# Kernel tuning notes

Measured on AMD Instinct MI355X. Metric: run time of the kernel, lower is better.

The kernel has to match this reference:

```python
import jax, jax.numpy as jnp
import numpy as np

N, D, C, P = 4096, 512, 100, 64
EPS_COS = 1e-8   # torch cosine_similarity norm clamp
EPS_INV = 1e-5   # module's 1/(d + 1e-5)


def setup_inputs() -> dict:
    key = jax.random.key(0)
    k1, k2, k3, k4 = jax.random.split(key, 4)
    feats = jax.random.normal(k1, (N, D), dtype=jnp.float32)
    protos = jax.random.normal(k2, (C, P, D), dtype=jnp.float32)
    cls_ids = jax.random.randint(k3, (N,), 0, C)
    proto_labels = jax.random.randint(k4, (C, P), 0, 1000)
    return {"feats": feats, "protos": protos, "cls_ids": cls_ids,
            "proto_labels": proto_labels}


def reference(feats, protos, cls_ids, proto_labels):
    # Gather each box's class-conditional prototype set: [N, P, D]
    p = protos[cls_ids]
    pl = proto_labels[cls_ids]                       # [N, P]

    # cosine distance: 1 - f.p / (max(|f|,eps) * max(|p|,eps))
    dot = jnp.einsum('nd,npd->np', feats, p)         # [N, P]
    fnorm = jnp.maximum(jnp.linalg.norm(feats, axis=-1, keepdims=True), EPS_COS)
    pnorm = jnp.maximum(jnp.linalg.norm(p, axis=-1), EPS_COS)
    d_cos = 1.0 - dot / (fnorm * pnorm)

    diff = feats[:, None, :] - p                     # [N, P, D]
    d_l1 = jnp.mean(jnp.abs(diff), axis=-1)          # F.l1_loss (mean)
    d_l2 = jnp.mean(diff * diff, axis=-1)            # F.mse_loss (mean)

    dists = jnp.stack([d_cos, d_l1, d_l2], axis=1)   # [N, 3, P]
    probs = jax.nn.softmax(1.0 / (dists + EPS_INV), axis=-1).mean(axis=1)  # [N, P]

    idx = jnp.argmax(probs, axis=-1)                 # [N]
    labels = jnp.take_along_axis(pl, idx[:, None], axis=1)[:, 0]
    return labels, probs
```

## Files before the change

kernel.cpp:

```cpp
#include <hip/hip_runtime.h>

#define D 512
#define P 64
#define WPB 4
#define EPS_COS 1e-8f
#define EPS_INV 1e-5f

__device__ __forceinline__ float wave_sum(float v) {
#pragma unroll
    for (int m = 32; m >= 1; m >>= 1) v += __shfl_xor(v, m, 64);
    return v;
}

__global__ __launch_bounds__(256) void proto_norm_kernel(
    const float* __restrict__ protos, float* __restrict__ pp, int rows)
{
    const int lane = threadIdx.x & 63;
    const int wave = threadIdx.x >> 6;
    const int r = blockIdx.x * WPB + wave;
    if (r >= rows) return;
    const float* row = protos + (size_t)r * D;
    const float4 a = *(const float4*)(row + lane * 4);
    const float4 b = *(const float4*)(row + 256 + lane * 4);
    float s = a.x*a.x + a.y*a.y + a.z*a.z + a.w*a.w
            + b.x*b.x + b.y*b.y + b.z*b.z + b.w*b.w;
    s = wave_sum(s);
    if (lane == 0) pp[r] = s;
}

__global__ __launch_bounds__(WPB * 64) void proto_probs_kernel(
    const float* __restrict__ feats,
    const float* __restrict__ protos,
    const int*   __restrict__ cls_ids,
    const int*   __restrict__ proto_labels,
    const float* __restrict__ ppbuf,
    float* __restrict__ out,
    int N)
{
    const int lane = threadIdx.x & 63;
    const int wave = threadIdx.x >> 6;
    const int n = blockIdx.x * WPB + wave;
    if (n >= N) return;

    const int cls = cls_ids[n];
    const float* f  = feats  + (size_t)n * D;
    const float* pr = protos + (size_t)cls * (P * D);

    const float4 f0 = *(const float4*)(f + lane * 4);
    const float4 f1 = *(const float4*)(f + 256 + lane * 4);

    float ff = f0.x*f0.x + f0.y*f0.y + f0.z*f0.z + f0.w*f0.w
             + f1.x*f1.x + f1.y*f1.y + f1.z*f1.z + f1.w*f1.w;
    ff = wave_sum(ff);

    const int jsel = (lane >> 3) & 7;
    const int gown = lane & 7;
    const bool hi32 = (lane & 32) != 0;
    const bool hi16 = (lane & 16) != 0;
    const bool hi8  = (lane & 8)  != 0;

    float r_dot = 0.f, r_l1 = 0.f;

    for (int g = 0; g < 8; ++g) {
        float pd[8], pl[8];
#pragma unroll
        for (int j = 0; j < 8; ++j) {
            const float* row = pr + (size_t)(8 * g + j) * D;
            const float4 q0 = *(const float4*)(row + lane * 4);
            const float4 q1 = *(const float4*)(row + 256 + lane * 4);
            float dot, l1, t;
            dot  = f0.x*q0.x; t = f0.x - q0.x; l1  = fabsf(t);
            dot += f0.y*q0.y; t = f0.y - q0.y; l1 += fabsf(t);
            dot += f0.z*q0.z; t = f0.z - q0.z; l1 += fabsf(t);
            dot += f0.w*q0.w; t = f0.w - q0.w; l1 += fabsf(t);
            dot += f1.x*q1.x; t = f1.x - q1.x; l1 += fabsf(t);
            dot += f1.y*q1.y; t = f1.y - q1.y; l1 += fabsf(t);
            dot += f1.z*q1.z; t = f1.z - q1.z; l1 += fabsf(t);
            dot += f1.w*q1.w; t = f1.w - q1.w; l1 += fabsf(t);
            pd[j] = dot; pl[j] = l1;
        }
#pragma unroll
        for (int k = 0; k < 4; ++k) {
            const float sd = hi32 ? pd[k] : pd[k + 4];
            const float sl = hi32 ? pl[k] : pl[k + 4];
            const float rd = __shfl_xor(sd, 32, 64);
            const float rl = __shfl_xor(sl, 32, 64);
            pd[k] = (hi32 ? pd[k + 4] : pd[k]) + rd;
            pl[k] = (hi32 ? pl[k + 4] : pl[k]) + rl;
        }
#pragma unroll
        for (int k = 0; k < 2; ++k) {
            const float sd = hi16 ? pd[k] : pd[k + 2];
            const float sl = hi16 ? pl[k] : pl[k + 2];
            const float rd = __shfl_xor(sd, 16, 64);
            const float rl = __shfl_xor(sl, 16, 64);
            pd[k] = (hi16 ? pd[k + 2] : pd[k]) + rd;
            pl[k] = (hi16 ? pl[k + 2] : pl[k]) + rl;
        }
        {
            const float sd = hi8 ? pd[0] : pd[1];
            const float sl = hi8 ? pl[0] : pl[1];
            const float rd = __shfl_xor(sd, 8, 64);
            const float rl = __shfl_xor(sl, 8, 64);
            pd[0] = (hi8 ? pd[1] : pd[0]) + rd;
            pl[0] = (hi8 ? pl[1] : pl[0]) + rl;
        }
#pragma unroll
        for (int m = 4; m >= 1; m >>= 1) {
            pd[0] += __shfl_xor(pd[0], m, 64);
            pl[0] += __shfl_xor(pl[0], m, 64);
        }
        if (gown == g) { r_dot = pd[0]; r_l1 = pl[0]; }
    }

    const int myp = 8 * gown + jsel;
    const float s_pp = ppbuf[cls * P + myp];

    const float fnorm = fmaxf(sqrtf(ff),   EPS_COS);
    const float pnorm = fmaxf(sqrtf(s_pp), EPS_COS);
    const float d_cos = 1.0f - r_dot / (fnorm * pnorm);
    const float d_l1  = r_l1 * (1.0f / (float)D);
    const float d_l2  = (ff - 2.0f * r_dot + s_pp) * (1.0f / (float)D);

    float s[3];
    s[0] = 1.0f / (d_cos + EPS_INV);
    s[1] = 1.0f / (d_l1  + EPS_INV);
    s[2] = 1.0f / (d_l2  + EPS_INV);

    float prob = 0.f;
#pragma unroll
    for (int i = 0; i < 3; ++i) {
        float m = s[i];
#pragma unroll
        for (int w = 32; w >= 1; w >>= 1) m = fmaxf(m, __shfl_xor(m, w, 64));
        const float e = expf(s[i] - m);
        const float denom = wave_sum(e);
        prob += e / denom;
    }
    prob *= (1.0f / 3.0f);

    float best = prob;
    int   bidx = myp;
#pragma unroll
    for (int w = 32; w >= 1; w >>= 1) {
        const float ov = __shfl_xor(best, w, 64);
        const int   oi = __shfl_xor(bidx, w, 64);
        if (ov > best || (ov == best && oi < bidx)) { best = ov; bidx = oi; }
    }

    out[(size_t)N + (size_t)n * P + myp] = prob;
    if (lane == 0) {
        out[n] = (float)proto_labels[cls * P + bidx];
    }
}

extern "C" void kernel_launch(void* const* d_in, const int* in_sizes, int n_in,
                              void* d_out, int out_size, void* d_ws, size_t ws_size,
                              hipStream_t stream) {
    const float* feats        = (const float*)d_in[0];
    const float* protos       = (const float*)d_in[1];
    const int*   cls_ids      = (const int*)d_in[2];
    const int*   proto_labels = (const int*)d_in[3];
    float* out = (float*)d_out;
    float* pp  = (float*)d_ws;

    const int N    = in_sizes[2];
    const int rows = in_sizes[1] / D;

    proto_norm_kernel<<<(rows + WPB - 1) / WPB, WPB * 64, 0, stream>>>(
        protos, pp, rows);
    proto_probs_kernel<<<(N + WPB - 1) / WPB, WPB * 64, 0, stream>>>(
        feats, protos, cls_ids, proto_labels, pp, out, N);
}
```

Baseline: 104.3 us.

## Bucket boxes by class and share prototype tiles in LDS across boxes

Adds a histogram, scan and scatter pipeline that groups boxes by class into chunks of up to 16. Each block then stages that class's 64 prototypes into shared memory in two passes and has each wave process 4 boxes against the staged tile, so every prototype load is reused 16 times instead of being re-read per box. The cost is four extra small launches, atomics and a 64 KB LDS tile per block, which limits occupancy. Chunks with fewer than 16 boxes leave some waves computing on padding, and the descriptor grid is fixed at 512 blocks.

```diff
diff --git a/kernel.cpp b/kernel.cpp
--- a/kernel.cpp
+++ b/kernel.cpp
@@ -2,10 +2,12 @@
 
 #define D 512
 #define P 64
-#define WPB 4
+#define CHUNK 16
+#define MAXDESC 512
 #define EPS_COS 1e-8f
 #define EPS_INV 1e-5f
 
+
 __device__ __forceinline__ float wave_sum(float v) {
 #pragma unroll
     for (int m = 32; m >= 1; m >>= 1) v += __shfl_xor(v, m, 64);
@@ -16,8 +18,7 @@
     const float* __restrict__ protos, float* __restrict__ pp, int rows)
 {
     const int lane = threadIdx.x & 63;
-    const int wave = threadIdx.x >> 6;
-    const int r = blockIdx.x * WPB + wave;
+    const int r = blockIdx.x * 4 + (threadIdx.x >> 6);
     if (r >= rows) return;
     const float* row = protos + (size_t)r * D;
     const float4 a = *(const float4*)(row + lane * 4);
@@ -28,129 +29,222 @@
     if (lane == 0) pp[r] = s;
 }
 
-__global__ __launch_bounds__(WPB * 64) void proto_probs_kernel(
+__global__ __launch_bounds__(256) void hist_kernel(
+    const int* __restrict__ cls, int* counts, int N)
+{
+    const int n = blockIdx.x * 256 + threadIdx.x;
+    if (n < N) atomicAdd(&counts[cls[n]], 1);
+}
+
+__global__ __launch_bounds__(64) void scan_desc_kernel(
+    const int* __restrict__ counts, int* base, int* desc, int* ndesc, int C)
+{
+    const int lane = threadIdx.x;
+    const int c0 = lane, c1 = lane + 64;
+    const int v0 = (c0 < C) ? counts[c0] : 0;
+    const int v1 = (c1 < C) ? counts[c1] : 0;
+    int s0 = v0, s1 = v1;
+#pragma unroll
+    for (int d = 1; d < 64; d <<= 1) {
+        int t = __shfl_up(s0, d, 64); if (lane >= d) s0 += t;
+        t     = __shfl_up(s1, d, 64); if (lane >= d) s1 += t;
+    }
+    s1 += __shfl(s0, 63, 64);
+    const int b0 = s0 - v0, b1 = s1 - v1;
+    if (c0 < C) base[c0] = b0;
+    if (c1 < C) base[c1] = b1;
+
+    const int g0 = (v0 + CHUNK - 1) / CHUNK, g1 = (v1 + CHUNK - 1) / CHUNK;
+    int t0 = g0, t1 = g1;
+#pragma unroll
+    for (int d = 1; d < 64; d <<= 1) {
+        int t = __shfl_up(t0, d, 64); if (lane >= d) t0 += t;
+        t     = __shfl_up(t1, d, 64); if (lane >= d) t1 += t;
+    }
+    t1 += __shfl(t0, 63, 64);
+    const int go0 = t0 - g0, go1 = t1 - g1;
+    if (lane == 63) ndesc[0] = t1;
+    for (int k = 0; k < g0; ++k) {
+        const int di = go0 + k;
+        desc[3*di] = c0; desc[3*di+1] = b0 + CHUNK*k; desc[3*di+2] = min(CHUNK, v0 - CHUNK*k);
+    }
+    for (int k = 0; k < g1; ++k) {
+        const int di = go1 + k;
+        desc[3*di] = c1; desc[3*di+1] = b1 + CHUNK*k; desc[3*di+2] = min(CHUNK, v1 - CHUNK*k);
+    }
+}
+
+__global__ __launch_bounds__(256) void scatter_kernel(
+    const int* __restrict__ cls, const int* __restrict__ base,
+    int* fill, int* sorted, int N)
+{
+    const int n = blockIdx.x * 256 + threadIdx.x;
+    if (n < N) {
+        const int c = cls[n];
+        const int pos = base[c] + atomicAdd(&fill[c], 1);
+        sorted[pos] = n;
+    }
+}
+
+__global__ __launch_bounds__(256, 2) void proto_main_kernel(
     const float* __restrict__ feats,
     const float* __restrict__ protos,
-    const int*   __restrict__ cls_ids,
     const int*   __restrict__ proto_labels,
     const float* __restrict__ ppbuf,
-    float* __restrict__ out,
-    int N)
-{
+    const int*   __restrict__ sorted,
+    const int*   __restrict__ desc,
+    const int*   __restrict__ ndesc,
+    float* __restrict__ out, int N)
+{
+    __shared__ float tile[32 * D];
+    const int nd = ndesc[0];
+    if ((int)blockIdx.x >= nd) return;
+    const int cls   = desc[3*blockIdx.x];
+    const int start = desc[3*blockIdx.x+1];
+    const int cnt   = desc[3*blockIdx.x+2];
     const int lane = threadIdx.x & 63;
     const int wave = threadIdx.x >> 6;
-    const int n = blockIdx.x * WPB + wave;
-    if (n >= N) return;
-
-    const int cls = cls_ids[n];
-    const float* f  = feats  + (size_t)n * D;
+
+    int  nidx[4];
+    bool valid[4];
+#pragma unroll
+    for (int k = 0; k < 4; ++k) {
+        const int pos = wave + 4*k;
+        valid[k] = pos < cnt;
+        nidx[k]  = sorted[start + (valid[k] ? pos : (cnt - 1))];
+    }
+
+    float4 f0[4], f1[4];
+    float  ff[4];
+#pragma unroll
+    for (int b = 0; b < 4; ++b) {
+        const float* f = feats + (size_t)nidx[b] * D;
+        f0[b] = *(const float4*)(f + lane * 4);
+        f1[b] = *(const float4*)(f + 256 + lane * 4);
+        float s = f0[b].x*f0[b].x + f0[b].y*f0[b].y + f0[b].z*f0[b].z + f0[b].w*f0[b].w
+                + f1[b].x*f1[b].x + f1[b].y*f1[b].y + f1[b].z*f1[b].z + f1[b].w*f1[b].w;
+        ff[b] = wave_sum(s);
+    }
+
     const float* pr = protos + (size_t)cls * (P * D);
-
-    const float4 f0 = *(const float4*)(f + lane * 4);
-    const float4 f1 = *(const float4*)(f + 256 + lane * 4);
-
-    float ff = f0.x*f0.x + f0.y*f0.y + f0.z*f0.z + f0.w*f0.w
-             + f1.x*f1.x + f1.y*f1.y + f1.z*f1.z + f1.w*f1.w;
-    ff = wave_sum(ff);
-
     const int jsel = (lane >> 3) & 7;
     const int gown = lane & 7;
     const bool hi32 = (lane & 32) != 0;
     const bool hi16 = (lane & 16) != 0;
     const bool hi8  = (lane & 8)  != 0;
 
-    float r_dot = 0.f, r_l1 = 0.f;
-
-    for (int g = 0; g < 8; ++g) {
-        float pd[8], pl[8];
-#pragma unroll
-        for (int j = 0; j < 8; ++j) {
-            const float* row = pr + (size_t)(8 * g + j) * D;
-            const float4 q0 = *(const float4*)(row + lane * 4);
-            const float4 q1 = *(const float4*)(row + 256 + lane * 4);
-            float dot, l1, t;
-            dot  = f0.x*q0.x; t = f0.x - q0.x; l1  = fabsf(t);
-            dot += f0.y*q0.y; t = f0.y - q0.y; l1 += fabsf(t);
-            dot += f0.z*q0.z; t = f0.z - q0.z; l1 += fabsf(t);
-            dot += f0.w*q0.w; t = f0.w - q0.w; l1 += fabsf(t);
-            dot += f1.x*q1.x; t = f1.x - q1.x; l1 += fabsf(t);
-            dot += f1.y*q1.y; t = f1.y - q1.y; l1 += fabsf(t);
-            dot += f1.z*q1.z; t = f1.z - q1.z; l1 += fabsf(t);
-            dot += f1.w*q1.w; t = f1.w - q1.w; l1 += fabsf(t);
-            pd[j] = dot; pl[j] = l1;
-        }
-#pragma unroll
-        for (int k = 0; k < 4; ++k) {
-            const float sd = hi32 ? pd[k] : pd[k + 4];
-            const float sl = hi32 ? pl[k] : pl[k + 4];
-            const float rd = __shfl_xor(sd, 32, 64);
-            const float rl = __shfl_xor(sl, 32, 64);
-            pd[k] = (hi32 ? pd[k + 4] : pd[k]) + rd;
-            pl[k] = (hi32 ? pl[k + 4] : pl[k]) + rl;
-        }
-#pragma unroll
-        for (int k = 0; k < 2; ++k) {
-            const float sd = hi16 ? pd[k] : pd[k + 2];
-            const float sl = hi16 ? pl[k] : pl[k + 2];
-            const float rd = __shfl_xor(sd, 16, 64);
-            const float rl = __shfl_xor(sl, 16, 64);
-            pd[k] = (hi16 ? pd[k + 2] : pd[k]) + rd;
-            pl[k] = (hi16 ? pl[k + 2] : pl[k]) + rl;
-        }
-        {
-            const float sd = hi8 ? pd[0] : pd[1];
-            const float sl = hi8 ? pl[0] : pl[1];
-            const float rd = __shfl_xor(sd, 8, 64);
-            const float rl = __shfl_xor(sl, 8, 64);
-            pd[0] = (hi8 ? pd[1] : pd[0]) + rd;
-            pl[0] = (hi8 ? pl[1] : pl[0]) + rl;
-        }
-#pragma unroll
-        for (int m = 4; m >= 1; m >>= 1) {
-            pd[0] += __shfl_xor(pd[0], m, 64);
-            pl[0] += __shfl_xor(pl[0], m, 64);
-        }
-        if (gown == g) { r_dot = pd[0]; r_l1 = pl[0]; }
+    float r_dot[4] = {0.f,0.f,0.f,0.f}, r_l1[4] = {0.f,0.f,0.f,0.f};
+
+    for (int pass = 0; pass < 2; ++pass) {
+#pragma unroll
+        for (int k = 0; k < 16; ++k) {
+            const int idx = threadIdx.x + 256 * k;
+            *(float4*)(tile + idx * 4) =
+                *(const float4*)(pr + pass * (32 * D) + idx * 4);
+        }
+        __syncthreads();
+
+        for (int gl = 0; gl < 4; ++gl) {
+            const int g = pass * 4 + gl;
+            float pd[4][8], pl[4][8];
+#pragma unroll
+            for (int j = 0; j < 8; ++j) {
+                const float* row = tile + (gl * 8 + j) * D;
+                const float4 q0 = *(const float4*)(row + lane * 4);
+                const float4 q1 = *(const float4*)(row + 256 + lane * 4);
+#pragma unroll
+                for (int b = 0; b < 4; ++b) {
+                    float dot, l1, t;
+                    dot  = f0[b].x*q0.x; t = f0[b].x - q0.x; l1  = fabsf(t);
+                    dot += f0[b].y*q0.y; t = f0[b].y - q0.y; l1 += fabsf(t);
+                    dot += f0[b].z*q0.z; t = f0[b].z - q0.z; l1 += fabsf(t);
+                    dot += f0[b].w*q0.w; t = f0[b].w - q0.w; l1 += fabsf(t);
+                    dot += f1[b].x*q1.x; t = f1[b].x - q1.x; l1 += fabsf(t);
+                    dot += f1[b].y*q1.y; t = f1[b].y - q1.y; l1 += fabsf(t);
+                    dot += f1[b].z*q1.z; t = f1[b].z - q1.z; l1 += fabsf(t);
+                    dot += f1[b].w*q1.w; t = f1[b].w - q1.w; l1 += fabsf(t);
+                    pd[b][j] = dot; pl[b][j] = l1;
+                }
+            }
+#pragma unroll
+            for (int b = 0; b < 4; ++b) {
+#pragma unroll
+                for (int k = 0; k < 4; ++k) {
+                    const float sd = hi32 ? pd[b][k] : pd[b][k+4];
+                    const float sl = hi32 ? pl[b][k] : pl[b][k+4];
+                    const float rd = __shfl_xor(sd, 32, 64);
+                    const float rl = __shfl_xor(sl, 32, 64);
+                    pd[b][k] = (hi32 ? pd[b][k+4] : pd[b][k]) + rd;
+                    pl[b][k] = (hi32 ? pl[b][k+4] : pl[b][k]) + rl;
+                }
+#pragma unroll
+                for (int k = 0; k < 2; ++k) {
+                    const float sd = hi16 ? pd[b][k] : pd[b][k+2];
+                    const float sl = hi16 ? pl[b][k] : pl[b][k+2];
+                    const float rd = __shfl_xor(sd, 16, 64);
+                    const float rl = __shfl_xor(sl, 16, 64);
+                    pd[b][k] = (hi16 ? pd[b][k+2] : pd[b][k]) + rd;
+                    pl[b][k] = (hi16 ? pl[b][k+2] : pl[b][k]) + rl;
+                }
+                {
+                    const float sd = hi8 ? pd[b][0] : pd[b][1];
+                    const float sl = hi8 ? pl[b][0] : pl[b][1];
+                    const float rd = __shfl_xor(sd, 8, 64);
+                    const float rl = __shfl_xor(sl, 8, 64);
+                    pd[b][0] = (hi8 ? pd[b][1] : pd[b][0]) + rd;
+                    pl[b][0] = (hi8 ? pl[b][1] : pl[b][0]) + rl;
+                }
+#pragma unroll
+                for (int m = 4; m >= 1; m >>= 1) {
+                    pd[b][0] += __shfl_xor(pd[b][0], m, 64);
+                    pl[b][0] += __shfl_xor(pl[b][0], m, 64);
+                }
+                if (gown == g) { r_dot[b] = pd[b][0]; r_l1[b] = pl[b][0]; }
+            }
+        }
+        __syncthreads();
     }
 
     const int myp = 8 * gown + jsel;
     const float s_pp = ppbuf[cls * P + myp];
 
-    const float fnorm = fmaxf(sqrtf(ff),   EPS_COS);
-    const float pnorm = fmaxf(sqrtf(s_pp), EPS_COS);
-    const float d_cos = 1.0f - r_dot / (fnorm * pnorm);
-    const float d_l1  = r_l1 * (1.0f / (float)D);
-    const float d_l2  = (ff - 2.0f * r_dot + s_pp) * (1.0f / (float)D);
-
-    float s[3];
-    s[0] = 1.0f / (d_cos + EPS_INV);
-    s[1] = 1.0f / (d_l1  + EPS_INV);
-    s[2] = 1.0f / (d_l2  + EPS_INV);
-
-    float prob = 0.f;
-#pragma unroll
-    for (int i = 0; i < 3; ++i) {
-        float m = s[i];
-#pragma unroll
-        for (int w = 32; w >= 1; w >>= 1) m = fmaxf(m, __shfl_xor(m, w, 64));
-        const float e = expf(s[i] - m);
-        const float denom = wave_sum(e);
-        prob += e / denom;
-    }
-    prob *= (1.0f / 3.0f);
-
-    float best = prob;
-    int   bidx = myp;
-#pragma unroll
-    for (int w = 32; w >= 1; w >>= 1) {
-        const float ov = __shfl_xor(best, w, 64);
-        const int   oi = __shfl_xor(bidx, w, 64);
-        if (ov > best || (ov == best && oi < bidx)) { best = ov; bidx = oi; }
-    }
-
-    out[(size_t)N + (size_t)n * P + myp] = prob;
-    if (lane == 0) {
-        out[n] = (float)proto_labels[cls * P + bidx];
+#pragma unroll
+    for (int b = 0; b < 4; ++b) {
+        const float fnorm = fmaxf(sqrtf(ff[b]), EPS_COS);
+        const float pnorm = fmaxf(sqrtf(s_pp),  EPS_COS);
+        const float d_cos = 1.0f - r_dot[b] / (fnorm * pnorm);
+        const float d_l1  = r_l1[b] * (1.0f / (float)D);
+        const float d_l2  = (ff[b] - 2.0f * r_dot[b] + s_pp) * (1.0f / (float)D);
+
+        float s[3];
+        s[0] = 1.0f / (d_cos + EPS_INV);
+        s[1] = 1.0f / (d_l1  + EPS_INV);
+        s[2] = 1.0f / (d_l2  + EPS_INV);
+
+        float prob = 0.f;
+#pragma unroll
+        for (int i = 0; i < 3; ++i) {
+            float m = s[i];
+#pragma unroll
+            for (int w = 32; w >= 1; w >>= 1) m = fmaxf(m, __shfl_xor(m, w, 64));
+            const float e = expf(s[i] - m);
+            prob += e / wave_sum(e);
+        }
+        prob *= (1.0f / 3.0f);
+
+        float best = prob;
+        int   bidx = myp;
+#pragma unroll
+        for (int w = 32; w >= 1; w >>= 1) {
+            const float ov = __shfl_xor(best, w, 64);
+            const int   oi = __shfl_xor(bidx, w, 64);
+            if (ov > best || (ov == best && oi < bidx)) { best = ov; bidx = oi; }
+        }
+
+        if (valid[b]) {
+            out[(size_t)N + (size_t)nidx[b] * P + myp] = prob;
+            if (lane == 0) out[nidx[b]] = (float)proto_labels[cls * P + bidx];
+        }
     }
 }
 
@@ -162,13 +256,25 @@
     const int*   cls_ids      = (const int*)d_in[2];
     const int*   proto_labels = (const int*)d_in[3];
     float* out = (float*)d_out;
-    float* pp  = (float*)d_ws;
 
     const int N    = in_sizes[2];
     const int rows = in_sizes[1] / D;
-
-    proto_norm_kernel<<<(rows + WPB - 1) / WPB, WPB * 64, 0, stream>>>(
-        protos, pp, rows);
-    proto_probs_kernel<<<(N + WPB - 1) / WPB, WPB * 64, 0, stream>>>(
-        feats, protos, cls_ids, proto_labels, pp, out, N);
-}
+    const int C    = rows / P;
+
+    char* w = (char*)d_ws;
+    float* pp     = (float*)w;
+    int*   counts = (int*)(w + 25600);
+    int*   fill   = (int*)(w + 26112);
+    int*   base   = (int*)(w + 26624);
+    int*   ndesc  = (int*)(w + 27136);
+    int*   desc   = (int*)(w + 27200);
+    int*   sorted = (int*)(w + 33344);
+
+    hipMemsetAsync(counts, 0, 1024, stream);
+    proto_norm_kernel<<<(rows + 3) / 4, 256, 0, stream>>>(protos, pp, rows);
+    hist_kernel<<<(N + 255) / 256, 256, 0, stream>>>(cls_ids, counts, N);
+    scan_desc_kernel<<<1, 64, 0, stream>>>(counts, base, desc, ndesc, C);
+    scatter_kernel<<<(N + 255) / 256, 256, 0, stream>>>(cls_ids, base, fill, sorted, N);
+    proto_main_kernel<<<MAXDESC, 256, 0, stream>>>(
+        feats, protos, proto_labels, pp, sorted, desc, ndesc, out, N);
+}
```

Result: slower. 128.1 us (+22.7%).
